# Optimization experiments

Hardware: AMD Instinct MI355X
Metric: run time of the kernel (lower is better)

The kernel has to match this reference:

```python
import jax, jax.numpy as jnp
import numpy as np

DT = 1.0          # config['IZHIK_TIME_STEP']
SURR_SCALE = 1.0  # ArcTan surrogate alpha
SURR_WIDTH = 20.0 # ArcTan surrogate width

@jax.custom_vjp
def spike_fn(x):
    # heaviside forward, ArcTan surrogate backward
    return (x > 0.0).astype(x.dtype)

def _spike_fwd(x):
    return spike_fn(x), x

def _spike_bwd(x, g):
    return (g * SURR_SCALE / (1.0 + (SURR_WIDTH * x) ** 2),)

spike_fn.defvjp(_spike_fwd, _spike_bwd)

B, T, N = 256, 500, 256

def setup_inputs() -> dict:
    key = jax.random.key(0)
    ks = jax.random.split(key, 14)
    input_batch = jax.random.normal(ks[0], (B, T, N), dtype=jnp.float32)
    state_snn = jnp.zeros((3, B, N), jnp.float32)   # (v, u, s)
    state_LI = jnp.zeros((B, 1), jnp.float32)
    W1 = jax.random.normal(ks[1], (N, N), jnp.float32) / np.sqrt(N)
    W2 = jax.random.normal(ks[2], (1, N), jnp.float32) / np.sqrt(N)
    def jit_param(k, base):
        return jnp.float32(base) * (1.0 + 0.1 * jax.random.uniform(k, (N,), jnp.float32))
    a      = jit_param(ks[3], 0.02)
    b      = jit_param(ks[4], 0.2)
    c      = jit_param(ks[5], -65.0)
    d      = jit_param(ks[6], 8.0)
    v0     = jit_param(ks[7], 140.0)
    v1     = jit_param(ks[8], 5.0)
    v2     = jit_param(ks[9], 0.04)
    tau_u  = jit_param(ks[10], 1.0)
    thresh = jit_param(ks[11], 30.0)
    leak   = jnp.full((1,), 0.9, jnp.float32)
    return dict(input_batch=input_batch, state_snn=state_snn, state_LI=state_LI,
                W1=W1, W2=W2, a=a, b=b, c=c, d=d, v0=v0, v1=v1, v2=v2,
                tau_u=tau_u, thresh=thresh, leak=leak)

def reference(input_batch, state_snn, state_LI, W1, W2, a, b, c, d, v0, v1, v2, tau_u, thresh, leak):
    x_seq = jnp.swapaxes(input_batch, 0, 1)  # [T, B, N]
    v_init, u_init, s_init = state_snn[0], state_snn[1], state_snn[2]

    def step(carry, x_t):
        v, u, s_prev, li = carry
        I = x_t @ W1.T                                        # [B, N] feedforward current
        v_mid = v + DT * (v2 * v * v + v1 * v + v0 - u + I)   # membrane update
        u_mid = u + (DT / tau_u) * a * (b * v - u)            # recovery update
        s = spike_fn(v_mid - thresh)                          # spike with surrogate grad
        v_new = v_mid * (1.0 - s) + s * c                     # reset v -> c on spike
        u_new = u_mid + s * d                                 # u += d on spike
        li_new = leak * li + (1.0 - leak) * (s @ W2.T)        # leaky-integrator readout [B,1]
        state_out = jnp.stack([v_new, u_new, s])              # [3, B, N]
        return (v_new, u_new, s, li_new), (s, state_out, li_new)

    _, (outputs, states_snn, decoded) = jax.lax.scan(
        step, (v_init, u_init, s_init, state_LI), x_seq)
    # outputs: [T, B, N]; states_snn: [T, 3, B, N]; decoded: [T, B, 1]
    return outputs, states_snn, decoded
```

## Files before the change

### kernel.cpp

```cpp
#include <hip/hip_runtime.h>

#define B_ 256
#define T_ 500
#define N_ 256
#define BN_ 65536
#define STP_ 196608
#define TW 64
#define NCHUNK 8

#define SOFT_BAR() do {                                   \
    __builtin_amdgcn_sched_barrier(0);                    \
    asm volatile("s_waitcnt lgkmcnt(0)" ::: "memory");    \
    __builtin_amdgcn_s_barrier();                         \
    __builtin_amdgcn_sched_barrier(0);                    \
} while (0)

__global__ __launch_bounds__(256)
void fused_snn_kernel(const float* __restrict__ X, const float* __restrict__ W1,
                      float* __restrict__ out_s, float* __restrict__ states,
                      float* __restrict__ out_dec,
                      const float* __restrict__ st_snn, const float* __restrict__ st_li,
                      const float* __restrict__ W2,
                      const float* __restrict__ pa, const float* __restrict__ pb,
                      const float* __restrict__ pc, const float* __restrict__ pd,
                      const float* __restrict__ pv0, const float* __restrict__ pv1,
                      const float* __restrict__ pv2, const float* __restrict__ ptau,
                      const float* __restrict__ pth, const float* __restrict__ pleak) {
    __shared__ float Al[TW * 256];
    __shared__ float Ws[2][16 * 256];
    __shared__ unsigned long long dotm[T_][4];
    __shared__ float dotf[T_][4];
    __shared__ float w2l[256];

    const int bb   = blockIdx.x;
    const int tid  = threadIdx.x;
    const int w    = tid >> 6;
    const int lane = tid & 63;
    const int boff = bb * 256 + tid;

    float v = st_snn[boff];
    float u = st_snn[BN_ + boff];
    const float a_   = pa[tid];
    const float b_   = pb[tid];
    const float c_   = pc[tid];
    const float d_   = pd[tid];
    const float v0_  = pv0[tid];
    const float v1_  = pv1[tid];
    const float v2_  = pv2[tid];
    const float coef = (1.0f / ptau[tid]) * a_;
    const float th_  = pth[tid];
    w2l[tid] = W2[tid];

    const int g   = tid >> 5;
    const int tg  = g << 3;
    const int h4  = (tid & 31) << 2;

    const float* Xb = X + (size_t)bb * (T_ * 256);
    const int tl = tid & 63;
    const int wq = (tid >> 6) << 2;

    const float* Wr0 = W1 + (size_t)tid * 256;
    const float4 z0 = *(const float4*)(Wr0 + 0);
    const float4 z1 = *(const float4*)(Wr0 + 4);
    const float4 z2 = *(const float4*)(Wr0 + 8);
    const float4 z3 = *(const float4*)(Wr0 + 12);

    float4 ra[16];
    {
        const int tsrc = ((tl < TW) ? tl : (TW - 1));
        const float* Xrow = Xb + (size_t)tsrc * 256;
#pragma unroll
        for (int r = 0; r < 16; ++r)
            ra[r] = *(const float4*)(Xrow + r * 16 + wq);
    }

    for (int cc = 0; cc < NCHUNK; ++cc) {
        const int t0    = cc * TW;
        const int valid = (T_ - t0 < TW) ? (T_ - t0) : TW;

#pragma unroll
        for (int r = 0; r < 16; ++r) {
            const int k = r * 16 + wq;
            Al[(k + 0) * 64 + tl] = ra[r].x;
            Al[(k + 1) * 64 + tl] = ra[r].y;
            Al[(k + 2) * 64 + tl] = ra[r].z;
            Al[(k + 3) * 64 + tl] = ra[r].w;
        }
        {
            float* Wd = &Ws[0][0];
            Wd[ 0*256+tid]=z0.x; Wd[ 1*256+tid]=z0.y; Wd[ 2*256+tid]=z0.z; Wd[ 3*256+tid]=z0.w;
            Wd[ 4*256+tid]=z1.x; Wd[ 5*256+tid]=z1.y; Wd[ 6*256+tid]=z1.z; Wd[ 7*256+tid]=z1.w;
            Wd[ 8*256+tid]=z2.x; Wd[ 9*256+tid]=z2.y; Wd[10*256+tid]=z2.z; Wd[11*256+tid]=z2.w;
            Wd[12*256+tid]=z3.x; Wd[13*256+tid]=z3.y; Wd[14*256+tid]=z3.z; Wd[15*256+tid]=z3.w;
        }
        SOFT_BAR();

        float acc[8][8];
#pragma unroll
        for (int i = 0; i < 8; ++i)
#pragma unroll
            for (int j = 0; j < 8; ++j) acc[i][j] = 0.f;

        for (int ks = 0; ks < 16; ++ks) {
            float4 w0, w1, w2v, w3;
            if (ks < 15) {
                const float* Wr = W1 + (size_t)tid * 256 + (ks + 1) * 16;
                w0 = *(const float4*)(Wr + 0);
                w1 = *(const float4*)(Wr + 4);
                w2v = *(const float4*)(Wr + 8);
                w3 = *(const float4*)(Wr + 12);
            }
            const float* Wc = &Ws[ks & 1][0];
            const int kbase = ks << 4;
#pragma unroll
            for (int kk = 0; kk < 16; ++kk) {
                const float4 a0 = *(const float4*)&Al[(kbase + kk) * 64 + tg];
                const float4 a1 = *(const float4*)&Al[(kbase + kk) * 64 + tg + 4];
                const float4 b0 = *(const float4*)&Wc[kk * 256 + h4];
                const float4 b1 = *(const float4*)&Wc[kk * 256 + h4 + 128];
                const float avr[8] = {a0.x, a0.y, a0.z, a0.w, a1.x, a1.y, a1.z, a1.w};
                const float bvr[8] = {b0.x, b0.y, b0.z, b0.w, b1.x, b1.y, b1.z, b1.w};
#pragma unroll
                for (int i = 0; i < 8; ++i)
#pragma unroll
                    for (int j = 0; j < 8; ++j)
                        acc[i][j] += avr[i] * bvr[j];
            }
            if (ks < 15) {
                float* Wd = &Ws[(ks + 1) & 1][0];
                Wd[ 0*256+tid]=w0.x; Wd[ 1*256+tid]=w0.y; Wd[ 2*256+tid]=w0.z; Wd[ 3*256+tid]=w0.w;
                Wd[ 4*256+tid]=w1.x; Wd[ 5*256+tid]=w1.y; Wd[ 6*256+tid]=w1.z; Wd[ 7*256+tid]=w1.w;
                Wd[ 8*256+tid]=w2v.x; Wd[ 9*256+tid]=w2v.y; Wd[10*256+tid]=w2v.z; Wd[11*256+tid]=w2v.w;
                Wd[12*256+tid]=w3.x; Wd[13*256+tid]=w3.y; Wd[14*256+tid]=w3.z; Wd[15*256+tid]=w3.w;
            }
            SOFT_BAR();
        }

#pragma unroll
        for (int i = 0; i < 8; ++i) {
            const int t = tg + i;
            *(float4*)&Al[t * 256 + h4] =
                make_float4(acc[i][0], acc[i][1], acc[i][2], acc[i][3]);
            *(float4*)&Al[t * 256 + h4 + 128] =
                make_float4(acc[i][4], acc[i][5], acc[i][6], acc[i][7]);
        }
        SOFT_BAR();

        if (cc + 1 < NCHUNK) {
            const int t0n    = (cc + 1) * TW;
            const int validn = (T_ - t0n < TW) ? (T_ - t0n) : TW;
            const int tsrc   = t0n + ((tl < validn) ? tl : (validn - 1));
            const float* Xrow = Xb + (size_t)tsrc * 256;
#pragma unroll
            for (int r = 0; r < 16; ++r)
                ra[r] = *(const float4*)(Xrow + r * 16 + wq);
        }

        {
            float Inx = Al[tid];
            for (int q = 0; q < valid; ++q) {
                const float Icur = Inx;
                if (q + 1 < valid) Inx = Al[(q + 1) * 256 + tid];
                const int t = t0 + q;
                const size_t pbase = (size_t)t * STP_ + boff;

                const float m1 = v2_ * v;
                const float t2 = v1_ * v;
                const float P  = __builtin_fmaf(m1, v, t2);
                const float Q  = (P + v0_) - u;
                const float vm = v + (Q + Icur);
                const float tb = __builtin_fmaf(b_, v, -u);
                const float um = __builtin_fmaf(coef, tb, u);

                const bool  sp = (vm - th_) > 0.f;
                const float s  = sp ? 1.f : 0.f;
                v = sp ? c_ : vm;
                u = sp ? (um + d_) : um;

                states[pbase]           = v;
                states[pbase + BN_]     = u;
                states[pbase + 2 * BN_] = s;
                out_s[(size_t)t * BN_ + boff] = s;

                const unsigned long long mset = __ballot(sp);
                if (lane == 0) dotm[t][w] = mset;
            }
        }
        SOFT_BAR();
    }

    for (int p = tid; p < T_ * 4; p += 256) {
        const int t  = p >> 2;
        const int ww = p & 3;
        unsigned long long m = dotm[t][ww];
        const float* wl = &w2l[ww << 6];
        float sum = 0.f;
        while (m) {
            const int i = __builtin_ctzll(m);
            sum += wl[i];
            m &= (m - 1);
        }
        dotf[t][ww] = sum;
    }
    __syncthreads();

    if (tid == 0) {
        const float lk_  = pleak[0];
        const float olk_ = 1.0f - lk_;
        float li = st_li[bb];
        for (int t = 0; t < T_; ++t) {
            const float dot = (dotf[t][0] + dotf[t][1]) + (dotf[t][2] + dotf[t][3]);
            li = lk_ * li + olk_ * dot;
            out_dec[(size_t)t * 256 + bb] = li;
        }
    }
}

extern "C" void kernel_launch(void* const* d_in, const int* in_sizes, int n_in,
                              void* d_out, int out_size, void* d_ws, size_t ws_size,
                              hipStream_t stream) {
    const float* input  = (const float*)d_in[0];
    const float* st_snn = (const float*)d_in[1];
    const float* st_li  = (const float*)d_in[2];
    const float* W1     = (const float*)d_in[3];
    const float* W2     = (const float*)d_in[4];
    const float* pa     = (const float*)d_in[5];
    const float* pb     = (const float*)d_in[6];
    const float* pc     = (const float*)d_in[7];
    const float* pd     = (const float*)d_in[8];
    const float* pv0    = (const float*)d_in[9];
    const float* pv1    = (const float*)d_in[10];
    const float* pv2    = (const float*)d_in[11];
    const float* ptau   = (const float*)d_in[12];
    const float* pth    = (const float*)d_in[13];
    const float* pleak  = (const float*)d_in[14];

    float* out        = (float*)d_out;
    float* out_s      = out;
    float* out_states = out + (size_t)T_ * BN_;
    float* out_dec    = out + (size_t)T_ * BN_ + (size_t)T_ * STP_;

    fused_snn_kernel<<<dim3(B_), dim3(256), 0, stream>>>(
        input, W1, out_s, out_states, out_dec, st_snn, st_li, W2,
        pa, pb, pc, pd, pv0, pv1, pv2, ptau, pth, pleak);
}
```

Baseline: 388.3 us.

## Overlap serial neuron recurrence of previous chunk with next chunk's GEMM

```diff
diff --git a/kernel.cpp b/kernel.cpp
--- a/kernel.cpp
+++ b/kernel.cpp
@@ -26,11 +26,10 @@
                       const float* __restrict__ pv0, const float* __restrict__ pv1,
                       const float* __restrict__ pv2, const float* __restrict__ ptau,
                       const float* __restrict__ pth, const float* __restrict__ pleak) {
-    __shared__ float Al[TW * 256];
-    __shared__ float Ws[2][16 * 256];
+    __shared__ float Xl[TW * 256];
+    __shared__ float Il[TW * 256];
+    __shared__ float Ws[2][8 * 256];
     __shared__ unsigned long long dotm[T_][4];
-    __shared__ float dotf[T_][4];
-    __shared__ float w2l[256];
 
     const int bb   = blockIdx.x;
     const int tid  = threadIdx.x;
@@ -49,7 +48,6 @@
     const float v2_  = pv2[tid];
     const float coef = (1.0f / ptau[tid]) * a_;
     const float th_  = pth[tid];
-    w2l[tid] = W2[tid];
 
     const int g   = tid >> 5;
     const int tg  = g << 3;
@@ -62,38 +60,33 @@
     const float* Wr0 = W1 + (size_t)tid * 256;
     const float4 z0 = *(const float4*)(Wr0 + 0);
     const float4 z1 = *(const float4*)(Wr0 + 4);
-    const float4 z2 = *(const float4*)(Wr0 + 8);
-    const float4 z3 = *(const float4*)(Wr0 + 12);
 
     float4 ra[16];
     {
-        const int tsrc = ((tl < TW) ? tl : (TW - 1));
-        const float* Xrow = Xb + (size_t)tsrc * 256;
+        const float* Xrow = Xb + (size_t)tl * 256;
 #pragma unroll
         for (int r = 0; r < 16; ++r)
             ra[r] = *(const float4*)(Xrow + r * 16 + wq);
     }
+#pragma unroll
+    for (int r = 0; r < 16; ++r) {
+        const int k = r * 16 + wq;
+        Xl[(k + 0) * 64 + tl] = ra[r].x;
+        Xl[(k + 1) * 64 + tl] = ra[r].y;
+        Xl[(k + 2) * 64 + tl] = ra[r].z;
+        Xl[(k + 3) * 64 + tl] = ra[r].w;
+    }
+    {
+        float* Wd = &Ws[0][0];
+        Wd[0*256+tid]=z0.x; Wd[1*256+tid]=z0.y; Wd[2*256+tid]=z0.z; Wd[3*256+tid]=z0.w;
+        Wd[4*256+tid]=z1.x; Wd[5*256+tid]=z1.y; Wd[6*256+tid]=z1.z; Wd[7*256+tid]=z1.w;
+    }
+    SOFT_BAR();
+
+    float Inx = 0.f;
 
     for (int cc = 0; cc < NCHUNK; ++cc) {
-        const int t0    = cc * TW;
-        const int valid = (T_ - t0 < TW) ? (T_ - t0) : TW;
-
-#pragma unroll
-        for (int r = 0; r < 16; ++r) {
-            const int k = r * 16 + wq;
-            Al[(k + 0) * 64 + tl] = ra[r].x;
-            Al[(k + 1) * 64 + tl] = ra[r].y;
-            Al[(k + 2) * 64 + tl] = ra[r].z;
-            Al[(k + 3) * 64 + tl] = ra[r].w;
-        }
-        {
-            float* Wd = &Ws[0][0];
-            Wd[ 0*256+tid]=z0.x; Wd[ 1*256+tid]=z0.y; Wd[ 2*256+tid]=z0.z; Wd[ 3*256+tid]=z0.w;
-            Wd[ 4*256+tid]=z1.x; Wd[ 5*256+tid]=z1.y; Wd[ 6*256+tid]=z1.z; Wd[ 7*256+tid]=z1.w;
-            Wd[ 8*256+tid]=z2.x; Wd[ 9*256+tid]=z2.y; Wd[10*256+tid]=z2.z; Wd[11*256+tid]=z2.w;
-            Wd[12*256+tid]=z3.x; Wd[13*256+tid]=z3.y; Wd[14*256+tid]=z3.z; Wd[15*256+tid]=z3.w;
-        }
-        SOFT_BAR();
+        const int tb = (cc - 1) * TW;
 
         float acc[8][8];
 #pragma unroll
@@ -101,21 +94,28 @@
 #pragma unroll
             for (int j = 0; j < 8; ++j) acc[i][j] = 0.f;
 
-        for (int ks = 0; ks < 16; ++ks) {
-            float4 w0, w1, w2v, w3;
-            if (ks < 15) {
-                const float* Wr = W1 + (size_t)tid * 256 + (ks + 1) * 16;
-                w0 = *(const float4*)(Wr + 0);
-                w1 = *(const float4*)(Wr + 4);
-                w2v = *(const float4*)(Wr + 8);
-                w3 = *(const float4*)(Wr + 12);
+        for (int ks = 0; ks < 32; ++ks) {
+            float4 q0, q1;
+            if (ks < 31) {
+                const float* Wr = W1 + (size_t)tid * 256 + (ks + 1) * 8;
+                q0 = *(const float4*)(Wr);
+                q1 = *(const float4*)(Wr + 4);
+            }
+            if (ks == 24 && cc + 1 < NCHUNK) {
+                const int t0n    = (cc + 1) * TW;
+                const int validn = (T_ - t0n < TW) ? (T_ - t0n) : TW;
+                const int tsrc   = t0n + ((tl < validn) ? tl : (validn - 1));
+                const float* Xrow = Xb + (size_t)tsrc * 256;
+#pragma unroll
+                for (int r = 0; r < 16; ++r)
+                    ra[r] = *(const float4*)(Xrow + r * 16 + wq);
             }
             const float* Wc = &Ws[ks & 1][0];
-            const int kbase = ks << 4;
-#pragma unroll
-            for (int kk = 0; kk < 16; ++kk) {
-                const float4 a0 = *(const float4*)&Al[(kbase + kk) * 64 + tg];
-                const float4 a1 = *(const float4*)&Al[(kbase + kk) * 64 + tg + 4];
+            const int kbase = ks << 3;
+#pragma unroll
+            for (int kk = 0; kk < 8; ++kk) {
+                const float4 a0 = *(const float4*)&Xl[(kbase + kk) * 64 + tg];
+                const float4 a1 = *(const float4*)&Xl[(kbase + kk) * 64 + tg + 4];
                 const float4 b0 = *(const float4*)&Wc[kk * 256 + h4];
                 const float4 b1 = *(const float4*)&Wc[kk * 256 + h4 + 128];
                 const float avr[8] = {a0.x, a0.y, a0.z, a0.w, a1.x, a1.y, a1.z, a1.w};
@@ -126,12 +126,41 @@
                     for (int j = 0; j < 8; ++j)
                         acc[i][j] += avr[i] * bvr[j];
             }
-            if (ks < 15) {
+            if (cc > 0) {
+#pragma unroll
+                for (int e = 0; e < 2; ++e) {
+                    const int q = (ks << 1) + e;
+                    const float Icur = Inx;
+                    if (q + 1 < TW) Inx = Il[(q + 1) * 256 + tid];
+                    const int t = tb + q;
+                    const size_t pbase = (size_t)t * STP_ + boff;
+
+                    const float m1 = v2_ * v;
+                    const float t2 = v1_ * v;
+                    const float P  = __builtin_fmaf(m1, v, t2);
+                    const float Q  = (P + v0_) - u;
+                    const float vm = v + (Q + Icur);
+                    const float tb2 = __builtin_fmaf(b_, v, -u);
+                    const float um = __builtin_fmaf(coef, tb2, u);
+
+                    const bool  sp = (vm - th_) > 0.f;
+                    const float s  = sp ? 1.f : 0.f;
+                    v = sp ? c_ : vm;
+                    u = sp ? (um + d_) : um;
+
+                    states[pbase]           = v;
+                    states[pbase + BN_]     = u;
+                    states[pbase + 2 * BN_] = s;
+                    out_s[(size_t)t * BN_ + boff] = s;
+
+                    const unsigned long long mset = __ballot(sp);
+                    if (lane == 0) dotm[t][w] = mset;
+                }
+            }
+            if (ks < 31) {
                 float* Wd = &Ws[(ks + 1) & 1][0];
-                Wd[ 0*256+tid]=w0.x; Wd[ 1*256+tid]=w0.y; Wd[ 2*256+tid]=w0.z; Wd[ 3*256+tid]=w0.w;
-                Wd[ 4*256+tid]=w1.x; Wd[ 5*256+tid]=w1.y; Wd[ 6*256+tid]=w1.z; Wd[ 7*256+tid]=w1.w;
-                Wd[ 8*256+tid]=w2v.x; Wd[ 9*256+tid]=w2v.y; Wd[10*256+tid]=w2v.z; Wd[11*256+tid]=w2v.w;
-                Wd[12*256+tid]=w3.x; Wd[13*256+tid]=w3.y; Wd[14*256+tid]=w3.z; Wd[15*256+tid]=w3.w;
+                Wd[0*256+tid]=q0.x; Wd[1*256+tid]=q0.y; Wd[2*256+tid]=q0.z; Wd[3*256+tid]=q0.w;
+                Wd[4*256+tid]=q1.x; Wd[5*256+tid]=q1.y; Wd[6*256+tid]=q1.z; Wd[7*256+tid]=q1.w;
             }
             SOFT_BAR();
         }
@@ -139,56 +168,65 @@
 #pragma unroll
         for (int i = 0; i < 8; ++i) {
             const int t = tg + i;
-            *(float4*)&Al[t * 256 + h4] =
+            *(float4*)&Il[t * 256 + h4] =
                 make_float4(acc[i][0], acc[i][1], acc[i][2], acc[i][3]);
-            *(float4*)&Al[t * 256 + h4 + 128] =
+            *(float4*)&Il[t * 256 + h4 + 128] =
                 make_float4(acc[i][4], acc[i][5], acc[i][6], acc[i][7]);
         }
+        if (cc + 1 < NCHUNK) {
+#pragma unroll
+            for (int r = 0; r < 16; ++r) {
+                const int k = r * 16 + wq;
+                Xl[(k + 0) * 64 + tl] = ra[r].x;
+                Xl[(k + 1) * 64 + tl] = ra[r].y;
+                Xl[(k + 2) * 64 + tl] = ra[r].z;
+                Xl[(k + 3) * 64 + tl] = ra[r].w;
+            }
+            float* Wd = &Ws[0][0];
+            Wd[0*256+tid]=z0.x; Wd[1*256+tid]=z0.y; Wd[2*256+tid]=z0.z; Wd[3*256+tid]=z0.w;
+            Wd[4*256+tid]=z1.x; Wd[5*256+tid]=z1.y; Wd[6*256+tid]=z1.z; Wd[7*256+tid]=z1.w;
+        }
         SOFT_BAR();
-
-        if (cc + 1 < NCHUNK) {
-            const int t0n    = (cc + 1) * TW;
-            const int validn = (T_ - t0n < TW) ? (T_ - t0n) : TW;
-            const int tsrc   = t0n + ((tl < validn) ? tl : (validn - 1));
-            const float* Xrow = Xb + (size_t)tsrc * 256;
-#pragma unroll
-            for (int r = 0; r < 16; ++r)
-                ra[r] = *(const float4*)(Xrow + r * 16 + wq);
-        }
-
-        {
-            float Inx = Al[tid];
-            for (int q = 0; q < valid; ++q) {
-                const float Icur = Inx;
-                if (q + 1 < valid) Inx = Al[(q + 1) * 256 + tid];
-                const int t = t0 + q;
-                const size_t pbase = (size_t)t * STP_ + boff;
-
-                const float m1 = v2_ * v;
-                const float t2 = v1_ * v;
-                const float P  = __builtin_fmaf(m1, v, t2);
-                const float Q  = (P + v0_) - u;
-                const float vm = v + (Q + Icur);
-                const float tb = __builtin_fmaf(b_, v, -u);
-                const float um = __builtin_fmaf(coef, tb, u);
-
-                const bool  sp = (vm - th_) > 0.f;
-                const float s  = sp ? 1.f : 0.f;
-                v = sp ? c_ : vm;
-                u = sp ? (um + d_) : um;
-
-                states[pbase]           = v;
-                states[pbase + BN_]     = u;
-                states[pbase + 2 * BN_] = s;
-                out_s[(size_t)t * BN_ + boff] = s;
-
-                const unsigned long long mset = __ballot(sp);
-                if (lane == 0) dotm[t][w] = mset;
-            }
-        }
-        SOFT_BAR();
-    }
-
+        Inx = Il[tid];
+    }
+
+    {
+        const int tbE = 7 * TW;
+        for (int q = 0; q < 52; ++q) {
+            const float Icur = Inx;
+            if (q + 1 < 52) Inx = Il[(q + 1) * 256 + tid];
+            const int t = tbE + q;
+            const size_t pbase = (size_t)t * STP_ + boff;
+
+            const float m1 = v2_ * v;
+            const float t2 = v1_ * v;
+            const float P  = __builtin_fmaf(m1, v, t2);
+            const float Q  = (P + v0_) - u;
+            const float vm = v + (Q + Icur);
+            const float tb2 = __builtin_fmaf(b_, v, -u);
+            const float um = __builtin_fmaf(coef, tb2, u);
+
+            const bool  sp = (vm - th_) > 0.f;
+            const float s  = sp ? 1.f : 0.f;
+            v = sp ? c_ : vm;
+            u = sp ? (um + d_) : um;
+
+            states[pbase]           = v;
+            states[pbase + BN_]     = u;
+            states[pbase + 2 * BN_] = s;
+            out_s[(size_t)t * BN_ + boff] = s;
+
+            const unsigned long long mset = __ballot(sp);
+            if (lane == 0) dotm[t][w] = mset;
+        }
+    }
+    __syncthreads();
+
+    float* scr  = &Ws[0][0];
+    float* w2l  = scr;
+    float* dotf = scr + 256;
+    w2l[tid] = W2[tid];
+    __syncthreads();
     for (int p = tid; p < T_ * 4; p += 256) {
         const int t  = p >> 2;
         const int ww = p & 3;
@@ -200,7 +238,7 @@
             sum += wl[i];
             m &= (m - 1);
         }
-        dotf[t][ww] = sum;
+        dotf[t * 4 + ww] = sum;
     }
     __syncthreads();
 
@@ -209,7 +247,7 @@
         const float olk_ = 1.0f - lk_;
         float li = st_li[bb];
         for (int t = 0; t < T_; ++t) {
-            const float dot = (dotf[t][0] + dotf[t][1]) + (dotf[t][2] + dotf[t][3]);
+            const float dot = (dotf[t*4+0] + dotf[t*4+1]) + (dotf[t*4+2] + dotf[t*4+3]);
             li = lk_ * li + olk_ * dot;
             out_dec[(size_t)t * 256 + bb] = li;
         }
```

Result: faster. 362.5 us, median of 2 (-6.6%).
